# Performance work log

Measured on AMD Instinct MI355X. Metric: run time of the kernel, lower is better.

## Reference

```python
import jax, jax.numpy as jnp
import numpy as np
from jax import lax

# --- static configuration (matches init_kwargs) ---
S = 128          # sheet_units
AK = 25          # aff_cf_units
AC = 1           # aff_cf_channels
AD = 1           # aff_cf_dilation
LK = 49          # lat_cf_units
LD = 1           # lat_cf_dilation
ITERS = 10       # lat_iters
EXC_RANGE = 5
TARGET_STRENGTH = 1.5
FM = 0.1         # float_mult

# --- helpers reconstructed from repo (radial cosine / circular masks) ---
def _rdist(size):
    c = (size - 1) / 2.0
    y, x = np.mgrid[0:size, 0:size]
    return np.sqrt((x - c) ** 2 + (y - c) ** 2)

def _circle(size, radius):
    return (_rdist(size) < radius).astype(np.float32)

def _rcos(size, radius):
    return np.cos(np.clip(_rdist(size) / radius, 0.0, 1.0) * np.pi / 2).astype(np.float32)

def _odd(n):
    return n if n % 2 == 1 else n + 1

# afferent connection-field envelope, flattened to (AC*AK*AK,)
_ae = _rcos(AK, AK) ** 2 * _circle(AK, AK / 2)
_ae = _ae / _ae.max()
AFF_ENV = jnp.asarray(np.tile(_ae.reshape(1, -1), (AC, 1)).reshape(-1))

# short-range excitation kernel (1,1,EXC,EXC), sums to 1
EXC = _odd(round(EXC_RANGE))
_s = _rcos(EXC, EXC_RANGE) ** 2 * _circle(EXC, EXC / 2)
SRE = jnp.asarray((_s / _s.sum()).reshape(1, 1, EXC, EXC))

# long-range inhibition envelope, flattened (LK*LK,)
_im = _rcos(LK, EXC / LD) ** 2 * _circle(LK, EXC / (2 * LD))
_le = _rcos(LK, LK) ** 2 * _circle(LK, LK / 2) * (1.0 - _im)
_le = _le.reshape(-1)
_le = _le / _le.max()
LRI_ENV = jnp.asarray(_le)

def _unfold(x, k, dilation, pad):
    # torch F.unfold equivalent -> (L, C*k*k) with channel-major patch flattening
    if pad:
        x = jnp.pad(x, ((0, 0), (0, 0), (pad, pad), (pad, pad)))
    p = lax.conv_general_dilated_patches(x, (k, k), (1, 1), 'VALID',
                                         rhs_dilation=(dilation, dilation))
    return p.reshape(p.shape[1], -1).T


def setup_inputs() -> dict:
    key = jax.random.key(0)
    k0, k1, k2 = jax.random.split(key, 3)
    x = jax.random.uniform(k0, (1, AC, S + AD * (AK - 1), S + AD * (AK - 1)), jnp.float32)
    rfs = jax.random.uniform(k1, (S * S, AC * AK * AK, 1), jnp.float32, minval=0.01, maxval=1.0)
    lat_weights = jax.random.uniform(k2, (S * S, LK * LK, 1), jnp.float32, minval=0.01, maxval=1.0)
    adathresh = jnp.zeros((1, 1, S, S), jnp.float32) + 0.1
    last_lat = jnp.zeros((1, 1, S, S), jnp.float32)
    lat_mean0 = jnp.zeros((1, 1, S, S), jnp.float32)
    return dict(x=x, rfs=rfs, lat_weights=lat_weights, adathresh=adathresh,
                last_lat=last_lat, lat_mean0=lat_mean0)


def reference(x, rfs, lat_weights, adathresh, last_lat, lat_mean0):
    sg = lax.stop_gradient
    Ka = rfs.shape[1]
    Kl = lat_weights.shape[1]
    # in-place no_grad weight normalisation (torch: param.data /= ...)
    rfs_n = rfs / sg(rfs.sum(1, keepdims=True) / (Ka * FM))
    lat_n = lat_weights / sg(lat_weights.sum(1, keepdims=True) / (Kl * FM))
    lat_w = sg(lat_n)[:, :, 0] / (Kl * FM)  # detached lateral weights (L, Kl)

    # afferent locally-connected projection
    x_tiles = _unfold(x, AK, max(1, round(AD)), 0) * AFF_ENV      # (L, Ka)
    raw_aff = jnp.einsum('lk,lk->l', x_tiles, rfs_n[:, :, 0]).reshape(1, 1, S, S)
    aff = sg(raw_aff) / (Ka * FM) - adathresh

    pad = (LK // 2) * LD
    ep = EXC // 2
    scaler = TARGET_STRENGTH

    def body(carry, _):
        lat, lm = carry
        latp = jnp.pad(lat, ((0, 0), (0, 0), (ep, ep), (ep, ep)), mode='reflect')
        lat_s = lax.conv_general_dilated(latp, SRE, (1, 1), 'VALID')  # (1,1,S,S)
        tiles = _unfold(lat_s, LK, LD, pad) * LRI_ENV                  # (L, Kl)
        lat_neg = jnp.einsum('lk,lk->l', tiles, lat_w).reshape(lat.shape)
        lat_new = jnp.maximum(lat_s + aff - 2.5 * lat_neg, 0.0) * 2.2
        lat_new = jnp.tanh(lat_new * scaler) / scaler
        lm = 0.5 * lm + 0.5 * lat_new
        return (lat_new, lm), None

    (lat, lat_mean), _ = lax.scan(body, (last_lat, lat_mean0), None, length=ITERS)

    # Hebbian lateral correlation term (learning_flag=True path)
    tiles_m = _unfold(lat_mean, LK, LD, pad) * LRI_ENV                 # (L, Kl)
    weighted = tiles_m * lat_mean.reshape(-1, 1)
    lat_correlations = jnp.einsum('lk,lk->', weighted, lat_n[:, :, 0])

    return raw_aff, lat, lat_correlations, x_tiles.reshape(S * S, 1, Ka)
```

## Files before the change

### kernel.cpp

```cpp
#include <hip/hip_runtime.h>
#include <math.h>

#define S 128
#define L (S*S)
#define AK 25
#define KA 625
#define LK 49
#define KL 2401
#define XW 152
#define PI2 1.57079632679489662f
#define MSCALE 1024.0f

typedef float v4f __attribute__((ext_vector_type(4)));
typedef _Float16 v4h __attribute__((ext_vector_type(4)));

#define WS_AENVD   0
#define WS_SRE     1024
#define WS_LRIRAW  2048
#define WS_LRID    5120
#define WS_AFF     8192
#define WS_LAT     40960
#define WS_LATS    57344
#define WS_LM      73728
#define WS_PART    90112
#define WS_M16     102400

#define OUT_LAT   16384
#define OUT_CORR  32768
#define OUT_XT    32769

__global__ __launch_bounds__(256) void init_consts(float* __restrict__ ws) {
    const int t = threadIdx.x;
    float* aenvd  = ws + WS_AENVD;
    float* sre    = ws + WS_SRE;
    float* lrraw  = ws + WS_LRIRAW;
    float* lrid   = ws + WS_LRID;
    __shared__ float red[256];

    for (int k = t; k < KA; k += 256) {
        int ky = k / AK, kx = k - ky * AK;
        float dy = (float)ky - 12.0f, dx = (float)kx - 12.0f;
        float rd = sqrtf(dx*dx + dy*dy);
        float c  = cosf(fminf(rd * (1.0f/25.0f), 1.0f) * PI2);
        aenvd[(k & 3) * 157 + (k >> 2)] = c*c * (rd < 12.5f ? 1.0f : 0.0f);
    }

    float myv = 0.0f;
    if (t < 25) {
        int ky = t / 5, kx = t - ky * 5;
        float dy = (float)ky - 2.0f, dx = (float)kx - 2.0f;
        float rd = sqrtf(dx*dx + dy*dy);
        float c  = cosf(fminf(rd * 0.2f, 1.0f) * PI2);
        myv = c*c * (rd < 2.5f ? 1.0f : 0.0f);
    }
    red[t] = myv;
    __syncthreads();
    for (int off = 128; off > 0; off >>= 1) {
        if (t < off) red[t] += red[t + off];
        __syncthreads();
    }
    float ssum = red[0];
    __syncthreads();
    if (t < 25) sre[t] = myv / ssum;

    float localmax = 0.0f;
    for (int k = t; k < KL; k += 256) {
        int ky = k / LK, kx = k - ky * LK;
        float dy = (float)ky - 24.0f, dx = (float)kx - 24.0f;
        float rd = sqrtf(dx*dx + dy*dy);
        float ci = cosf(fminf(rd * 0.2f, 1.0f) * PI2);
        float im = ci*ci * (rd < 2.5f ? 1.0f : 0.0f);
        float co = cosf(fminf(rd * (1.0f/49.0f), 1.0f) * PI2);
        float le = co*co * (rd < 24.5f ? 1.0f : 0.0f) * (1.0f - im);
        lrraw[k] = le;
        localmax = fmaxf(localmax, le);
    }
    red[t] = localmax;
    __syncthreads();
    for (int off = 128; off > 0; off >>= 1) {
        if (t < off) red[t] = fmaxf(red[t], red[t + off]);
        __syncthreads();
    }
    float invm = 1.0f / red[0];
    __syncthreads();
    for (int k = t; k < KL; k += 256)
        lrid[(k & 3) * 601 + (k >> 2)] = lrraw[k] * invm;
}

__global__ __launch_bounds__(256) void prep_kernel(
    const float* __restrict__ lw, const float* __restrict__ lri_d,
    _Float16* __restrict__ m16)
{
    __shared__ float lriS[2404];
    const int tid = threadIdx.x;
    const int wave = tid >> 6, lane = tid & 63;
    for (int i = tid; i < 2404; i += 256) lriS[i] = lri_d[i];
    __syncthreads();

    const int unit = blockIdx.x * 4 + wave;
    const int base = unit * KL;
    const int h = (-base) & 3;
    const int tl = (base + KL) & 3;
    const int m4 = (KL - h - tl) >> 2;
    const int rem = m4 - 576;

    const v4f* w4p = (const v4f*)(lw + base + h);
    v4f wv[9];
    #pragma unroll
    for (int i = 0; i < 9; i++) wv[i] = w4p[lane + (i << 6)];
    v4f wv9 = (v4f)(0.0f);
    bool has9 = lane < rem;
    if (has9) wv9 = w4p[576 + lane];
    float whd = 0.0f, wtl = 0.0f;
    if (lane < h)  whd = lw[base + lane];
    if (lane < tl) wtl = lw[base + KL - tl + lane];

    float wsum = whd + wtl;
    #pragma unroll
    for (int i = 0; i < 9; i++) wsum += wv[i][0] + wv[i][1] + wv[i][2] + wv[i][3];
    wsum += wv9[0] + wv9[1] + wv9[2] + wv9[3];
    #pragma unroll
    for (int off = 1; off < 64; off <<= 1) wsum += __shfl_xor(wsum, off);
    const float scale = MSCALE / wsum;

    v4h* m4p = (v4h*)(m16 + base + h);
    if (lane < h)
        m16[base + lane] = (_Float16)(whd * lriS[(lane & 3) * 601 + (lane >> 2)] * scale);
    if (lane < tl) {
        int k = KL - tl + lane;
        m16[base + k] = (_Float16)(wtl * lriS[(k & 3) * 601 + (k >> 2)] * scale);
    }
    #pragma unroll
    for (int i = 0; i < 9; i++) {
        int q = lane + (i << 6);
        int kq = h + (q << 2);
        v4h st;
        #pragma unroll
        for (int e = 0; e < 4; e++) {
            int k = kq + e;
            st[e] = (_Float16)(wv[i][e] * lriS[(k & 3) * 601 + (k >> 2)] * scale);
        }
        m4p[q] = st;
    }
    if (has9) {
        int q = 576 + lane;
        int kq = h + (q << 2);
        v4h st;
        #pragma unroll
        for (int e = 0; e < 4; e++) {
            int k = kq + e;
            st[e] = (_Float16)(wv9[e] * lriS[(k & 3) * 601 + (k >> 2)] * scale);
        }
        m4p[q] = st;
    }
}

__global__ __launch_bounds__(256) void aff_kernel(
    const float* __restrict__ x, const float* __restrict__ rfs,
    const float* __restrict__ ada, const float* __restrict__ aenv_d,
    float* __restrict__ raw_aff_out, float* __restrict__ xtiles_out,
    float* __restrict__ aff_ws)
{
    __shared__ float xwin[700];
    __shared__ float env[628];
    const int tid = threadIdx.x;
    const int wave = tid >> 6, lane = tid & 63;
    const int unit0 = blockIdx.x * 4;
    const int r0 = unit0 >> 7, c0 = unit0 & 127;

    for (int i = tid; i < 628; i += 256) env[i] = aenv_d[i];
    for (int i = tid; i < 700; i += 256) {
        int wy = i / 28, wx = i - wy * 28;
        xwin[(i & 3) * 175 + (i >> 2)] = x[(r0 + wy) * XW + c0 + wx];
    }
    __syncthreads();

    const int unit = unit0 + wave;
    const int base = unit * KA;
    const int h = (-base) & 3;
    const int tl = (base + KA) & 3;
    const int m4 = (KA - h - tl) >> 2;
    const int rem = m4 - 128;

    const v4f* w4p = (const v4f*)(rfs + base + h);
    v4f wv0 = w4p[lane];
    v4f wv1 = w4p[lane + 64];
    v4f wv2 = (v4f)(0.0f);
    bool has2 = lane < rem;
    if (has2) wv2 = w4p[128 + lane];
    float wh = 0.0f, wt = 0.0f;
    if (lane < h)  wh = rfs[base + lane];
    if (lane < tl) wt = rfs[base + KA - tl + lane];

    float* trow = xtiles_out + (size_t)unit * KA;
    v4f* t4p = (v4f*)(trow + h);
    float adot = 0.0f, rsum = 0.0f;

    if (lane < h) {
        int j = lane + wave;
        float xt = xwin[(j & 3) * 175 + (j >> 2)] * env[(lane & 3) * 157 + (lane >> 2)];
        trow[lane] = xt;
        adot = fmaf(xt, wh, adot); rsum += wh;
    }
    if (lane < tl) {
        int k = KA - tl + lane;
        int ky = (int)(((unsigned)k * 83887u) >> 21);
        int j = k + 3 * ky + wave;
        float xt = xwin[(j & 3) * 175 + (j >> 2)] * env[(k & 3) * 157 + (k >> 2)];
        trow[k] = xt;
        adot = fmaf(xt, wt, adot); rsum += wt;
    }
    #pragma unroll
    for (int i = 0; i < 2; i++) {
        v4f wq = (i == 0) ? wv0 : wv1;
        int q = lane + (i << 6);
        int kq = h + (q << 2);
        v4f st;
        #pragma unroll
        for (int e = 0; e < 4; e++) {
            int k = kq + e;
            int ky = (int)(((unsigned)k * 83887u) >> 21);
            int j = k + 3 * ky + wave;
            float xt = xwin[(j & 3) * 175 + (j >> 2)] * env[(k & 3) * 157 + (k >> 2)];
            st[e] = xt;
            adot = fmaf(xt, wq[e], adot);
            rsum += wq[e];
        }
        __builtin_nontemporal_store(st, &t4p[q]);
    }
    if (has2) {
        int q = 128 + lane;
        int kq = h + (q << 2);
        v4f st;
        #pragma unroll
        for (int e = 0; e < 4; e++) {
            int k = kq + e;
            int ky = (int)(((unsigned)k * 83887u) >> 21);
            int j = k + 3 * ky + wave;
            float xt = xwin[(j & 3) * 175 + (j >> 2)] * env[(k & 3) * 157 + (k >> 2)];
            st[e] = xt;
            adot = fmaf(xt, wv2[e], adot);
            rsum += wv2[e];
        }
        __builtin_nontemporal_store(st, &t4p[q]);
    }

    for (int off = 32; off > 0; off >>= 1) {
        adot += __shfl_down(adot, off);
        rsum += __shfl_down(rsum, off);
    }
    if (lane == 0) {
        float inv = 1.0f / rsum;
        raw_aff_out[unit] = 62.5f * adot * inv;
        aff_ws[unit] = adot * inv - ada[unit];
    }
}

__global__ __launch_bounds__(256) void smooth_kernel(
    const float* __restrict__ lat, const float* __restrict__ sre,
    float* __restrict__ lat_s)
{
    const int idx = blockIdx.x * 256 + threadIdx.x;
    const int r = idx >> 7, c = idx & 127;
    float acc = 0.0f;
    #pragma unroll
    for (int a = 0; a < 5; a++) {
        int rr = r + a - 2;
        rr = rr < 0 ? -rr : (rr > 127 ? 254 - rr : rr);
        #pragma unroll
        for (int b = 0; b < 5; b++) {
            int cc = c + b - 2;
            cc = cc < 0 ? -cc : (cc > 127 ? 254 - cc : cc);
            acc = fmaf(sre[a * 5 + b], lat[rr * 128 + cc], acc);
        }
    }
    lat_s[idx] = acc;
}

__global__ __launch_bounds__(256) void lat_kernel(
    const _Float16* __restrict__ m16, const float* __restrict__ lat_s,
    const float* __restrict__ aff, const float* __restrict__ lm_in,
    float* __restrict__ lm_out, float* __restrict__ lat_out,
    float* __restrict__ lat_final)
{
    __shared__ float win[2548];
    const int tid = threadIdx.x;
    const int wave = tid >> 6, lane = tid & 63;
    const int unit0 = blockIdx.x * 4;
    const int r0 = unit0 >> 7, c0 = unit0 & 127;

    for (int i = tid; i < 2548; i += 256) {
        int wy = i / 52, wx = i - wy * 52;
        int rr = r0 - 24 + wy, cc = c0 - 24 + wx;
        float v = 0.0f;
        if (rr >= 0 && rr < 128 && cc >= 0 && cc < 128) v = lat_s[rr * 128 + cc];
        win[(i & 3) * 637 + (i >> 2)] = v;
    }
    __syncthreads();

    const int unit = unit0 + wave;
    const int base = unit * KL;
    const int h = (-base) & 3;
    const int tl = (base + KL) & 3;
    const int m4 = (KL - h - tl) >> 2;
    const int rem = m4 - 576;

    const v4h* m4p = (const v4h*)(m16 + base + h);
    v4h wv[9];
    #pragma unroll
    for (int i = 0; i < 9; i++) wv[i] = m4p[lane + (i << 6)];
    v4h wv9 = (v4h)((_Float16)0.0f);
    bool has9 = lane < rem;
    if (has9) wv9 = m4p[576 + lane];
    float whd = 0.0f, wtl = 0.0f;
    if (lane < h)  whd = (float)m16[base + lane];
    if (lane < tl) wtl = (float)m16[base + KL - tl + lane];

    float dot = 0.0f;
    if (lane < h) {
        int rr = lane + wave;
        dot = fmaf(whd, win[(rr & 3) * 637 + (rr >> 2)], dot);
    }
    if (lane < tl) {
        int k = KL - tl + lane;
        int ky = (int)(((unsigned)k * 42800u) >> 21);
        int rr = k + 3 * ky + wave;
        dot = fmaf(wtl, win[(rr & 3) * 637 + (rr >> 2)], dot);
    }
    #pragma unroll
    for (int i = 0; i < 9; i++) {
        int kq = h + ((lane + (i << 6)) << 2);
        #pragma unroll
        for (int e = 0; e < 4; e++) {
            int k = kq + e;
            int ky = (int)(((unsigned)k * 42800u) >> 21);
            int rr = k + 3 * ky + wave;
            dot = fmaf((float)wv[i][e], win[(rr & 3) * 637 + (rr >> 2)], dot);
        }
    }
    if (has9) {
        int kq = h + ((576 + lane) << 2);
        #pragma unroll
        for (int e = 0; e < 4; e++) {
            int k = kq + e;
            int ky = (int)(((unsigned)k * 42800u) >> 21);
            int rr = k + 3 * ky + wave;
            dot = fmaf((float)wv9[e], win[(rr & 3) * 637 + (rr >> 2)], dot);
        }
    }

    for (int off = 32; off > 0; off >>= 1) dot += __shfl_down(dot, off);
    if (lane == 0) {
        int rc = 24 * 52 + 24 + wave;
        float ls = win[(rc & 3) * 637 + (rc >> 2)];
        float ln = fmaxf(ls + aff[unit] - (2.5f / MSCALE) * dot, 0.0f) * 2.2f;
        ln = tanhf(ln * 1.5f) * (1.0f / 1.5f);
        float lm = 0.5f * lm_in[unit] + 0.5f * ln;
        lm_out[unit] = lm;
        lat_out[unit] = ln;
        if (lat_final) lat_final[unit] = ln;
    }
}

__global__ __launch_bounds__(256) void hebb_kernel(
    const _Float16* __restrict__ m16, const float* __restrict__ lm,
    float* __restrict__ partials)
{
    __shared__ float win[2548];
    __shared__ float wred[4];
    const int tid = threadIdx.x;
    const int wave = tid >> 6, lane = tid & 63;
    const int unit0 = blockIdx.x * 4;
    const int r0 = unit0 >> 7, c0 = unit0 & 127;

    for (int i = tid; i < 2548; i += 256) {
        int wy = i / 52, wx = i - wy * 52;
        int rr = r0 - 24 + wy, cc = c0 - 24 + wx;
        float v = 0.0f;
        if (rr >= 0 && rr < 128 && cc >= 0 && cc < 128) v = lm[rr * 128 + cc];
        win[(i & 3) * 637 + (i >> 2)] = v;
    }
    __syncthreads();

    const int unit = unit0 + wave;
    const int base = unit * KL;
    const int h = (-base) & 3;
    const int tl = (base + KL) & 3;
    const int m4 = (KL - h - tl) >> 2;
    const int rem = m4 - 576;

    const v4h* m4p = (const v4h*)(m16 + base + h);
    v4h wv[9];
    #pragma unroll
    for (int i = 0; i < 9; i++) wv[i] = m4p[lane + (i << 6)];
    v4h wv9 = (v4h)((_Float16)0.0f);
    bool has9 = lane < rem;
    if (has9) wv9 = m4p[576 + lane];
    float whd = 0.0f, wtl = 0.0f;
    if (lane < h)  whd = (float)m16[base + lane];
    if (lane < tl) wtl = (float)m16[base + KL - tl + lane];

    float dot = 0.0f;
    if (lane < h) {
        int rr = lane + wave;
        dot = fmaf(whd, win[(rr & 3) * 637 + (rr >> 2)], dot);
    }
    if (lane < tl) {
        int k = KL - tl + lane;
        int ky = (int)(((unsigned)k * 42800u) >> 21);
        int rr = k + 3 * ky + wave;
        dot = fmaf(wtl, win[(rr & 3) * 637 + (rr >> 2)], dot);
    }
    #pragma unroll
    for (int i = 0; i < 9; i++) {
        int kq = h + ((lane + (i << 6)) << 2);
        #pragma unroll
        for (int e = 0; e < 4; e++) {
            int k = kq + e;
            int ky = (int)(((unsigned)k * 42800u) >> 21);
            int rr = k + 3 * ky + wave;
            dot = fmaf((float)wv[i][e], win[(rr & 3) * 637 + (rr >> 2)], dot);
        }
    }
    if (has9) {
        int kq = h + ((576 + lane) << 2);
        #pragma unroll
        for (int e = 0; e < 4; e++) {
            int k = kq + e;
            int ky = (int)(((unsigned)k * 42800u) >> 21);
            int rr = k + 3 * ky + wave;
            dot = fmaf((float)wv9[e], win[(rr & 3) * 637 + (rr >> 2)], dot);
        }
    }
    for (int off = 32; off > 0; off >>= 1) dot += __shfl_down(dot, off);
    if (lane == 0) {
        int rc = 24 * 52 + 24 + wave;
        float center = win[(rc & 3) * 637 + (rc >> 2)];
        wred[wave] = center * (240.1f / MSCALE) * dot;
    }
    __syncthreads();
    if (tid == 0) partials[blockIdx.x] = wred[0] + wred[1] + wred[2] + wred[3];
}

__global__ __launch_bounds__(256) void reduce_kernel(
    const float* __restrict__ partials, float* __restrict__ out)
{
    __shared__ float red[256];
    float s = 0.0f;
    for (int i = threadIdx.x; i < 4096; i += 256) s += partials[i];
    red[threadIdx.x] = s;
    __syncthreads();
    for (int off = 128; off > 0; off >>= 1) {
        if (threadIdx.x < off) red[threadIdx.x] += red[threadIdx.x + off];
        __syncthreads();
    }
    if (threadIdx.x == 0) out[0] = red[0];
}

extern "C" void kernel_launch(void* const* d_in, const int* in_sizes, int n_in,
                              void* d_out, int out_size, void* d_ws, size_t ws_size,
                              hipStream_t stream) {
    const float* x        = (const float*)d_in[0];
    const float* rfs      = (const float*)d_in[1];
    const float* lw       = (const float*)d_in[2];
    const float* ada      = (const float*)d_in[3];
    const float* last_lat = (const float*)d_in[4];
    const float* lm0      = (const float*)d_in[5];
    float* out = (float*)d_out;
    float* ws  = (float*)d_ws;
    _Float16* m16 = (_Float16*)(ws + WS_M16);

    init_consts<<<1, 256, 0, stream>>>(ws);
    aff_kernel<<<L / 4, 256, 0, stream>>>(x, rfs, ada, ws + WS_AENVD,
                                          out, out + OUT_XT, ws + WS_AFF);
    prep_kernel<<<L / 4, 256, 0, stream>>>(lw, ws + WS_LRID, m16);
    for (int it = 0; it < 10; ++it) {
        const float* lat_in = (it == 0) ? last_lat : (ws + WS_LAT);
        const float* lmsrc  = (it == 0) ? lm0 : (ws + WS_LM);
        smooth_kernel<<<L / 256, 256, 0, stream>>>(lat_in, ws + WS_SRE, ws + WS_LATS);
        lat_kernel<<<L / 4, 256, 0, stream>>>(m16, ws + WS_LATS, ws + WS_AFF,
                                              lmsrc, ws + WS_LM, ws + WS_LAT,
                                              (it == 9) ? (out + OUT_LAT) : nullptr);
    }
    hebb_kernel<<<L / 4, 256, 0, stream>>>(m16, ws + WS_LM, ws + WS_PART);
    reduce_kernel<<<1, 256, 0, stream>>>(ws + WS_PART, out + OUT_CORR);
}
```

Baseline: 560.2 us.

## Fuse smoothing into lateral kernel with padded fp16 weight layout and 4x4 unit tiles

Stores the fp16 lateral weights in a padded 52-wide row layout so lanes use aligned 8-wide loads without head/tail handling. Folds the 5x5 reflect-padded smoothing into the lateral kernel, and has each block compute a 4x4 unit tile so the shared window is reused across 16 units. The next unit's weights are prefetched while the current dot product runs. The separate reduce kernel is replaced by an atomicAdd into a zeroed output, and lat buffers are ping-ponged so the fused kernel does not race on its input. Each block recomputes the smoothed window redundantly, raises shared-memory use, and the atomic reduction order is non-deterministic.

```diff
diff --git a/kernel.cpp b/kernel.cpp
--- a/kernel.cpp
+++ b/kernel.cpp
@@ -7,22 +7,22 @@
 #define KA 625
 #define LK 49
 #define KL 2401
+#define KJ 2552
 #define XW 152
 #define PI2 1.57079632679489662f
 #define MSCALE 1024.0f
 
 typedef float v4f __attribute__((ext_vector_type(4)));
-typedef _Float16 v4h __attribute__((ext_vector_type(4)));
+typedef _Float16 v8h __attribute__((ext_vector_type(8)));
 
 #define WS_AENVD   0
-#define WS_SRE     1024
-#define WS_LRIRAW  2048
-#define WS_LRID    5120
+#define WS_SRE     640
+#define WS_LRID    672
+#define WS_LRIRAW  4096
 #define WS_AFF     8192
-#define WS_LAT     40960
-#define WS_LATS    57344
+#define WS_LATA    40960
+#define WS_LATB    57344
 #define WS_LM      73728
-#define WS_PART    90112
 #define WS_M16     102400
 
 #define OUT_LAT   16384
@@ -98,60 +98,35 @@
     __syncthreads();
 
     const int unit = blockIdx.x * 4 + wave;
-    const int base = unit * KL;
-    const int h = (-base) & 3;
-    const int tl = (base + KL) & 3;
-    const int m4 = (KL - h - tl) >> 2;
-    const int rem = m4 - 576;
-
-    const v4f* w4p = (const v4f*)(lw + base + h);
-    v4f wv[9];
-    #pragma unroll
-    for (int i = 0; i < 9; i++) wv[i] = w4p[lane + (i << 6)];
-    v4f wv9 = (v4f)(0.0f);
-    bool has9 = lane < rem;
-    if (has9) wv9 = w4p[576 + lane];
-    float whd = 0.0f, wtl = 0.0f;
-    if (lane < h)  whd = lw[base + lane];
-    if (lane < tl) wtl = lw[base + KL - tl + lane];
-
-    float wsum = whd + wtl;
-    #pragma unroll
-    for (int i = 0; i < 9; i++) wsum += wv[i][0] + wv[i][1] + wv[i][2] + wv[i][3];
-    wsum += wv9[0] + wv9[1] + wv9[2] + wv9[3];
+    const float* wrow = lw + (size_t)unit * KL;
+
+    float wsum = 0.0f;
+    for (int i = lane; i < KL; i += 64) wsum += wrow[i];
     #pragma unroll
     for (int off = 1; off < 64; off <<= 1) wsum += __shfl_xor(wsum, off);
     const float scale = MSCALE / wsum;
 
-    v4h* m4p = (v4h*)(m16 + base + h);
-    if (lane < h)
-        m16[base + lane] = (_Float16)(whd * lriS[(lane & 3) * 601 + (lane >> 2)] * scale);
-    if (lane < tl) {
-        int k = KL - tl + lane;
-        m16[base + k] = (_Float16)(wtl * lriS[(k & 3) * 601 + (k >> 2)] * scale);
-    }
-    #pragma unroll
-    for (int i = 0; i < 9; i++) {
-        int q = lane + (i << 6);
-        int kq = h + (q << 2);
-        v4h st;
-        #pragma unroll
-        for (int e = 0; e < 4; e++) {
-            int k = kq + e;
-            st[e] = (_Float16)(wv[i][e] * lriS[(k & 3) * 601 + (k >> 2)] * scale);
+    v8h* orow = (v8h*)(m16 + (size_t)unit * KJ);
+    #pragma unroll
+    for (int i = 0; i < 5; i++) {
+        const int q = lane + (i << 6);
+        if (q < 319) {
+            const int j0 = q << 3;
+            v8h st;
+            #pragma unroll
+            for (int e = 0; e < 8; e++) {
+                const int j = j0 + e;
+                const int ky = (int)(((unsigned)j * 40330u) >> 21);
+                const int kx = j - 52 * ky;
+                float w = 0.0f;
+                if (kx < 49) {
+                    const int k = j - 3 * ky;
+                    w = wrow[k] * lriS[(k & 3) * 601 + (k >> 2)] * scale;
+                }
+                st[e] = (_Float16)w;
+            }
+            orow[q] = st;
         }
-        m4p[q] = st;
-    }
-    if (has9) {
-        int q = 576 + lane;
-        int kq = h + (q << 2);
-        v4h st;
-        #pragma unroll
-        for (int e = 0; e < 4; e++) {
-            int k = kq + e;
-            st[e] = (_Float16)(wv9[e] * lriS[(k & 3) * 601 + (k >> 2)] * scale);
-        }
-        m4p[q] = st;
     }
 }
 
@@ -159,7 +134,7 @@
     const float* __restrict__ x, const float* __restrict__ rfs,
     const float* __restrict__ ada, const float* __restrict__ aenv_d,
     float* __restrict__ raw_aff_out, float* __restrict__ xtiles_out,
-    float* __restrict__ aff_ws)
+    float* __restrict__ aff_ws, float* __restrict__ corr)
 {
     __shared__ float xwin[700];
     __shared__ float env[628];
@@ -167,6 +142,8 @@
     const int wave = tid >> 6, lane = tid & 63;
     const int unit0 = blockIdx.x * 4;
     const int r0 = unit0 >> 7, c0 = unit0 & 127;
+
+    if (blockIdx.x == 0 && tid == 0) corr[0] = 0.0f;
 
     for (int i = tid; i < 628; i += 256) env[i] = aenv_d[i];
     for (int i = tid; i < 700; i += 256) {
@@ -256,205 +233,153 @@
     }
 }
 
-__global__ __launch_bounds__(256) void smooth_kernel(
-    const float* __restrict__ lat, const float* __restrict__ sre,
-    float* __restrict__ lat_s)
-{
-    const int idx = blockIdx.x * 256 + threadIdx.x;
-    const int r = idx >> 7, c = idx & 127;
-    float acc = 0.0f;
-    #pragma unroll
-    for (int a = 0; a < 5; a++) {
-        int rr = r + a - 2;
-        rr = rr < 0 ? -rr : (rr > 127 ? 254 - rr : rr);
-        #pragma unroll
-        for (int b = 0; b < 5; b++) {
-            int cc = c + b - 2;
-            cc = cc < 0 ? -cc : (cc > 127 ? 254 - cc : cc);
-            acc = fmaf(sre[a * 5 + b], lat[rr * 128 + cc], acc);
-        }
-    }
-    lat_s[idx] = acc;
+#define LOADW(P, W0, W1, W2, W3, W4) \
+    v8h W0 = (P)[lane]; v8h W1 = (P)[lane + 64]; v8h W2 = (P)[lane + 128]; \
+    v8h W3 = (P)[lane + 192]; v8h W4 = (v8h)(_Float16)0.0f; \
+    if (lane < 63) W4 = (P)[256 + lane];
+
+__device__ __forceinline__ float dot_row(v8h w0, v8h w1, v8h w2, v8h w3, v8h w4,
+                                         int lane, int woff, const float* win)
+{
+    float dot = 0.0f;
+    const int a0 = lane << 1;
+    #pragma unroll
+    for (int e = 0; e < 8; e++) {
+        const int c = woff + e;
+        const int ae = a0 + (c & 3) * 676 + (c >> 2);
+        dot = fmaf((float)w0[e], win[ae],       dot);
+        dot = fmaf((float)w1[e], win[ae + 128], dot);
+        dot = fmaf((float)w2[e], win[ae + 256], dot);
+        dot = fmaf((float)w3[e], win[ae + 384], dot);
+        dot = fmaf((float)w4[e], win[ae + 512], dot);
+    }
+    return dot;
+}
+
+__device__ __forceinline__ void lat_epi(float dot, int lane, int wave, int du,
+    int unit, const float* win, const float* __restrict__ aff,
+    const float* __restrict__ lm_in, float* __restrict__ lm_out,
+    float* __restrict__ lat_out, float* __restrict__ lat_final)
+{
+    #pragma unroll
+    for (int off = 32; off > 0; off >>= 1) dot += __shfl_down(dot, off);
+    if (lane == 0) {
+        const int ci = (24 + wave) * 52 + 24 + du;
+        const float ls = win[(ci & 3) * 676 + (ci >> 2)];
+        float ln = fmaxf(ls + aff[unit] - (2.5f / MSCALE) * dot, 0.0f) * 2.2f;
+        ln = tanhf(ln * 1.5f) * (1.0f / 1.5f);
+        lm_out[unit] = 0.5f * lm_in[unit] + 0.5f * ln;
+        lat_out[unit] = ln;
+        if (lat_final) lat_final[unit] = ln;
+    }
 }
 
 __global__ __launch_bounds__(256) void lat_kernel(
-    const _Float16* __restrict__ m16, const float* __restrict__ lat_s,
-    const float* __restrict__ aff, const float* __restrict__ lm_in,
-    float* __restrict__ lm_out, float* __restrict__ lat_out,
-    float* __restrict__ lat_final)
-{
-    __shared__ float win[2548];
+    const _Float16* __restrict__ m16, const float* __restrict__ lat_in,
+    const float* __restrict__ sre_g, const float* __restrict__ aff,
+    const float* __restrict__ lm_in, float* __restrict__ lm_out,
+    float* __restrict__ lat_out, float* __restrict__ lat_final)
+{
+    __shared__ float raw[3136];
+    __shared__ float win[2708];
     const int tid = threadIdx.x;
     const int wave = tid >> 6, lane = tid & 63;
-    const int unit0 = blockIdx.x * 4;
-    const int r0 = unit0 >> 7, c0 = unit0 & 127;
-
-    for (int i = tid; i < 2548; i += 256) {
-        int wy = i / 52, wx = i - wy * 52;
-        int rr = r0 - 24 + wy, cc = c0 - 24 + wx;
+    const int r0 = (blockIdx.x >> 5) << 2, c0 = (blockIdx.x & 31) << 2;
+
+    for (int i = tid; i < 3136; i += 256) {
+        int wy = i / 56, wx = i - wy * 56;
+        int ar = r0 - 26 + wy; ar = ar < 0 ? -ar : (ar > 127 ? 254 - ar : ar);
+        int ac = c0 - 26 + wx; ac = ac < 0 ? -ac : (ac > 127 ? 254 - ac : ac);
+        raw[i] = lat_in[ar * 128 + ac];
+    }
+    if (tid < 4) win[2704 + tid] = 0.0f;
+
+    float sr[25];
+    #pragma unroll
+    for (int j = 0; j < 25; j++) sr[j] = sre_g[j];
+
+    const int urow = r0 + wave;
+    const v8h* p8 = (const v8h*)(m16 + (size_t)(urow * 128 + c0) * KJ);
+    LOADW(p8, a0w, a1w, a2w, a3w, a4w)
+
+    __syncthreads();
+
+    for (int i = tid; i < 2704; i += 256) {
+        int wr = i / 52, wc = i - wr * 52;
+        int arr = r0 - 24 + wr, acl = c0 - 24 + wc;
         float v = 0.0f;
-        if (rr >= 0 && rr < 128 && cc >= 0 && cc < 128) v = lat_s[rr * 128 + cc];
-        win[(i & 3) * 637 + (i >> 2)] = v;
-    }
-    __syncthreads();
-
-    const int unit = unit0 + wave;
-    const int base = unit * KL;
-    const int h = (-base) & 3;
-    const int tl = (base + KL) & 3;
-    const int m4 = (KL - h - tl) >> 2;
-    const int rem = m4 - 576;
-
-    const v4h* m4p = (const v4h*)(m16 + base + h);
-    v4h wv[9];
-    #pragma unroll
-    for (int i = 0; i < 9; i++) wv[i] = m4p[lane + (i << 6)];
-    v4h wv9 = (v4h)((_Float16)0.0f);
-    bool has9 = lane < rem;
-    if (has9) wv9 = m4p[576 + lane];
-    float whd = 0.0f, wtl = 0.0f;
-    if (lane < h)  whd = (float)m16[base + lane];
-    if (lane < tl) wtl = (float)m16[base + KL - tl + lane];
-
-    float dot = 0.0f;
-    if (lane < h) {
-        int rr = lane + wave;
-        dot = fmaf(whd, win[(rr & 3) * 637 + (rr >> 2)], dot);
-    }
-    if (lane < tl) {
-        int k = KL - tl + lane;
-        int ky = (int)(((unsigned)k * 42800u) >> 21);
-        int rr = k + 3 * ky + wave;
-        dot = fmaf(wtl, win[(rr & 3) * 637 + (rr >> 2)], dot);
-    }
-    #pragma unroll
-    for (int i = 0; i < 9; i++) {
-        int kq = h + ((lane + (i << 6)) << 2);
-        #pragma unroll
-        for (int e = 0; e < 4; e++) {
-            int k = kq + e;
-            int ky = (int)(((unsigned)k * 42800u) >> 21);
-            int rr = k + 3 * ky + wave;
-            dot = fmaf((float)wv[i][e], win[(rr & 3) * 637 + (rr >> 2)], dot);
+        if (((unsigned)arr < 128u) && ((unsigned)acl < 128u)) {
+            const float* rp = raw + wr * 56 + wc;
+            float a = 0.0f;
+            #pragma unroll
+            for (int ay = 0; ay < 5; ay++)
+                #pragma unroll
+                for (int bx = 0; bx < 5; bx++)
+                    a = fmaf(sr[ay * 5 + bx], rp[ay * 56 + bx], a);
+            v = a;
         }
-    }
-    if (has9) {
-        int kq = h + ((576 + lane) << 2);
-        #pragma unroll
-        for (int e = 0; e < 4; e++) {
-            int k = kq + e;
-            int ky = (int)(((unsigned)k * 42800u) >> 21);
-            int rr = k + 3 * ky + wave;
-            dot = fmaf((float)wv9[e], win[(rr & 3) * 637 + (rr >> 2)], dot);
-        }
-    }
-
-    for (int off = 32; off > 0; off >>= 1) dot += __shfl_down(dot, off);
-    if (lane == 0) {
-        int rc = 24 * 52 + 24 + wave;
-        float ls = win[(rc & 3) * 637 + (rc >> 2)];
-        float ln = fmaxf(ls + aff[unit] - (2.5f / MSCALE) * dot, 0.0f) * 2.2f;
-        ln = tanhf(ln * 1.5f) * (1.0f / 1.5f);
-        float lm = 0.5f * lm_in[unit] + 0.5f * ln;
-        lm_out[unit] = lm;
-        lat_out[unit] = ln;
-        if (lat_final) lat_final[unit] = ln;
-    }
+        win[(i & 3) * 676 + (i >> 2)] = v;
+    }
+    __syncthreads();
+
+    const int woff = wave * 52;
+    const int ub = urow * 128 + c0;
+
+    const v8h* q1 = (const v8h*)(m16 + (size_t)(ub + 1) * KJ);
+    LOADW(q1, b0w, b1w, b2w, b3w, b4w)
+    float d0 = dot_row(a0w, a1w, a2w, a3w, a4w, lane, woff + 0, win);
+    const v8h* q2 = (const v8h*)(m16 + (size_t)(ub + 2) * KJ);
+    LOADW(q2, c0w, c1w, c2w, c3w, c4w)
+    lat_epi(d0, lane, wave, 0, ub + 0, win, aff, lm_in, lm_out, lat_out, lat_final);
+    float d1 = dot_row(b0w, b1w, b2w, b3w, b4w, lane, woff + 1, win);
+    const v8h* q3 = (const v8h*)(m16 + (size_t)(ub + 3) * KJ);
+    LOADW(q3, e0w, e1w, e2w, e3w, e4w)
+    lat_epi(d1, lane, wave, 1, ub + 1, win, aff, lm_in, lm_out, lat_out, lat_final);
+    float d2 = dot_row(c0w, c1w, c2w, c3w, c4w, lane, woff + 2, win);
+    lat_epi(d2, lane, wave, 2, ub + 2, win, aff, lm_in, lm_out, lat_out, lat_final);
+    float d3 = dot_row(e0w, e1w, e2w, e3w, e4w, lane, woff + 3, win);
+    lat_epi(d3, lane, wave, 3, ub + 3, win, aff, lm_in, lm_out, lat_out, lat_final);
 }
 
 __global__ __launch_bounds__(256) void hebb_kernel(
     const _Float16* __restrict__ m16, const float* __restrict__ lm,
-    float* __restrict__ partials)
-{
-    __shared__ float win[2548];
+    float* __restrict__ corr)
+{
+    __shared__ float win[2708];
     __shared__ float wred[4];
     const int tid = threadIdx.x;
     const int wave = tid >> 6, lane = tid & 63;
-    const int unit0 = blockIdx.x * 4;
-    const int r0 = unit0 >> 7, c0 = unit0 & 127;
-
-    for (int i = tid; i < 2548; i += 256) {
-        int wy = i / 52, wx = i - wy * 52;
-        int rr = r0 - 24 + wy, cc = c0 - 24 + wx;
+    const int r0 = (blockIdx.x >> 5) << 2, c0 = (blockIdx.x & 31) << 2;
+
+    for (int i = tid; i < 2704; i += 256) {
+        int wr = i / 52, wc = i - wr * 52;
+        int ar = r0 - 24 + wr, ac = c0 - 24 + wc;
         float v = 0.0f;
-        if (rr >= 0 && rr < 128 && cc >= 0 && cc < 128) v = lm[rr * 128 + cc];
-        win[(i & 3) * 637 + (i >> 2)] = v;
-    }
-    __syncthreads();
-
-    const int unit = unit0 + wave;
-    const int base = unit * KL;
-    const int h = (-base) & 3;
-    const int tl = (base + KL) & 3;
-    const int m4 = (KL - h - tl) >> 2;
-    const int rem = m4 - 576;
-
-    const v4h* m4p = (const v4h*)(m16 + base + h);
-    v4h wv[9];
-    #pragma unroll
-    for (int i = 0; i < 9; i++) wv[i] = m4p[lane + (i << 6)];
-    v4h wv9 = (v4h)((_Float16)0.0f);
-    bool has9 = lane < rem;
-    if (has9) wv9 = m4p[576 + lane];
-    float whd = 0.0f, wtl = 0.0f;
-    if (lane < h)  whd = (float)m16[base + lane];
-    if (lane < tl) wtl = (float)m16[base + KL - tl + lane];
-
-    float dot = 0.0f;
-    if (lane < h) {
-        int rr = lane + wave;
-        dot = fmaf(whd, win[(rr & 3) * 637 + (rr >> 2)], dot);
-    }
-    if (lane < tl) {
-        int k = KL - tl + lane;
-        int ky = (int)(((unsigned)k * 42800u) >> 21);
-        int rr = k + 3 * ky + wave;
-        dot = fmaf(wtl, win[(rr & 3) * 637 + (rr >> 2)], dot);
-    }
-    #pragma unroll
-    for (int i = 0; i < 9; i++) {
-        int kq = h + ((lane + (i << 6)) << 2);
+        if (((unsigned)ar < 128u) && ((unsigned)ac < 128u)) v = lm[ar * 128 + ac];
+        win[(i & 3) * 676 + (i >> 2)] = v;
+    }
+    if (tid < 4) win[2704 + tid] = 0.0f;
+    __syncthreads();
+
+    const int urow = r0 + wave;
+    const int woff = wave * 52;
+    float bsum = 0.0f;
+    #pragma unroll
+    for (int du = 0; du < 4; ++du) {
+        const v8h* p = (const v8h*)(m16 + (size_t)(urow * 128 + c0 + du) * KJ);
+        LOADW(p, w0, w1, w2, w3, w4)
+        float d = dot_row(w0, w1, w2, w3, w4, lane, woff + du, win);
         #pragma unroll
-        for (int e = 0; e < 4; e++) {
-            int k = kq + e;
-            int ky = (int)(((unsigned)k * 42800u) >> 21);
-            int rr = k + 3 * ky + wave;
-            dot = fmaf((float)wv[i][e], win[(rr & 3) * 637 + (rr >> 2)], dot);
+        for (int off = 32; off > 0; off >>= 1) d += __shfl_down(d, off);
+        if (lane == 0) {
+            const int ci = (24 + wave) * 52 + 24 + du;
+            bsum = fmaf(win[(ci & 3) * 676 + (ci >> 2)], d, bsum);
         }
     }
-    if (has9) {
-        int kq = h + ((576 + lane) << 2);
-        #pragma unroll
-        for (int e = 0; e < 4; e++) {
-            int k = kq + e;
-            int ky = (int)(((unsigned)k * 42800u) >> 21);
-            int rr = k + 3 * ky + wave;
-            dot = fmaf((float)wv9[e], win[(rr & 3) * 637 + (rr >> 2)], dot);
-        }
-    }
-    for (int off = 32; off > 0; off >>= 1) dot += __shfl_down(dot, off);
-    if (lane == 0) {
-        int rc = 24 * 52 + 24 + wave;
-        float center = win[(rc & 3) * 637 + (rc >> 2)];
-        wred[wave] = center * (240.1f / MSCALE) * dot;
-    }
-    __syncthreads();
-    if (tid == 0) partials[blockIdx.x] = wred[0] + wred[1] + wred[2] + wred[3];
-}
-
-__global__ __launch_bounds__(256) void reduce_kernel(
-    const float* __restrict__ partials, float* __restrict__ out)
-{
-    __shared__ float red[256];
-    float s = 0.0f;
-    for (int i = threadIdx.x; i < 4096; i += 256) s += partials[i];
-    red[threadIdx.x] = s;
-    __syncthreads();
-    for (int off = 128; off > 0; off >>= 1) {
-        if (threadIdx.x < off) red[threadIdx.x] += red[threadIdx.x + off];
-        __syncthreads();
-    }
-    if (threadIdx.x == 0) out[0] = red[0];
+    if (lane == 0) wred[wave] = bsum;
+    __syncthreads();
+    if (tid == 0)
+        atomicAdd(corr, (wred[0] + wred[1] + wred[2] + wred[3]) * (240.1f / MSCALE));
 }
 
 extern "C" void kernel_launch(void* const* d_in, const int* in_sizes, int n_in,
@@ -472,16 +397,18 @@
 
     init_consts<<<1, 256, 0, stream>>>(ws);
     aff_kernel<<<L / 4, 256, 0, stream>>>(x, rfs, ada, ws + WS_AENVD,
-                                          out, out + OUT_XT, ws + WS_AFF);
+                                          out, out + OUT_XT, ws + WS_AFF, out + OUT_CORR);
     prep_kernel<<<L / 4, 256, 0, stream>>>(lw, ws + WS_LRID, m16);
+
+    float* bufA = ws + WS_LATA;
+    float* bufB = ws + WS_LATB;
     for (int it = 0; it < 10; ++it) {
-        const float* lat_in = (it == 0) ? last_lat : (ws + WS_LAT);
-        const float* lmsrc  = (it == 0) ? lm0 : (ws + WS_LM);
-        smooth_kernel<<<L / 256, 256, 0, stream>>>(lat_in, ws + WS_SRE, ws + WS_LATS);
-        lat_kernel<<<L / 4, 256, 0, stream>>>(m16, ws + WS_LATS, ws + WS_AFF,
-                                              lmsrc, ws + WS_LM, ws + WS_LAT,
-                                              (it == 9) ? (out + OUT_LAT) : nullptr);
-    }
-    hebb_kernel<<<L / 4, 256, 0, stream>>>(m16, ws + WS_LM, ws + WS_PART);
-    reduce_kernel<<<1, 256, 0, stream>>>(ws + WS_PART, out + OUT_CORR);
-}
+        const float* lat_in = (it == 0) ? last_lat : ((it & 1) ? bufA : bufB);
+        float* lat_out = (it & 1) ? bufB : bufA;
+        const float* lmsrc = (it == 0) ? lm0 : (ws + WS_LM);
+        lat_kernel<<<1024, 256, 0, stream>>>(m16, lat_in, ws + WS_SRE, ws + WS_AFF,
+                                             lmsrc, ws + WS_LM, lat_out,
+                                             (it == 9) ? (out + OUT_LAT) : nullptr);
+    }
+    hebb_kernel<<<1024, 256, 0, stream>>>(m16, ws + WS_LM, out + OUT_CORR);
+}
```

Result: no change. 564.7 us (+0.8%).
